# Performance work log

Hardware: AMD Instinct MI355X
Metric: run time of the kernel (lower is better)

Reference implementation:

```python
import jax, jax.numpy as jnp
import numpy as np

N_NODES = 50000
N_EDGES = 800000
D = 128
SAME_W = 0.3
CROSS_W = 1.0


def setup_inputs() -> dict:
    key = jax.random.key(0)
    k1, k2, k3, k4, k5 = jax.random.split(key, 5)
    x = jax.random.normal(k1, (N_NODES, D), dtype=jnp.float32)
    edge_index = jax.random.randint(k2, (2, N_EDGES), 0, N_NODES, dtype=jnp.int64)
    edge_weight = jax.random.uniform(k3, (N_EDGES,), dtype=jnp.float32)
    Wr1 = jax.random.normal(k4, (D, D), dtype=jnp.float32) * (1.0 / np.sqrt(D))
    Wr2 = jax.random.normal(k5, (D, D), dtype=jnp.float32) * (1.0 / np.sqrt(D))
    return {"x": x, "edge_index": edge_index, "edge_weight": edge_weight,
            "Wr1": Wr1, "Wr2": Wr2, "cell_len": 20000}


def _node_types(idx, cell_len):
    # get_node_types: type 0 if idx <= cell_len, else 1 (note the <=, faithful to source)
    return (idx > cell_len).astype(jnp.int32)


def _conv_layer(x, src, dst, per_edge_w, Wr, n_nodes):
    # gather -> weight -> scatter-mean -> + root linear
    msg = x[src] * per_edge_w[:, None]                       # [E, D]
    agg = jax.ops.segment_sum(msg, dst, num_segments=n_nodes)  # [N, D]
    cnt = jax.ops.segment_sum(jnp.ones_like(per_edge_w), dst, num_segments=n_nodes)
    agg = agg / jnp.maximum(cnt, 1.0)[:, None]               # mean aggr (0 if no edges)
    return agg + x @ Wr.T                                     # lin_r, bias=False


def reference(x, edge_index, edge_weight, Wr1, Wr2, cell_len):
    src, dst = edge_index[0], edge_index[1]
    same = _node_types(src, cell_len) == _node_types(dst, cell_len)
    type_w = jnp.where(same, SAME_W, CROSS_W).astype(x.dtype)
    w = type_w * edge_weight                                  # [E]
    n_nodes = x.shape[0]
    h = _conv_layer(x, src, dst, w, Wr1, n_nodes)
    out = _conv_layer(h, src, dst, w, Wr2, n_nodes)
    return out
```

## Files before the change

### kernel.cpp

```cpp
#include <hip/hip_runtime.h>
#include <cstdint>
#include <cstddef>

#define D 128
#define SAME_W 0.3f
#define CROSS_W 1.0f
#define NSLICE 8
#define CAP 64
#define GEMM_BLOCKS 1024

using bf16x8 = __attribute__((ext_vector_type(8))) __bf16;
using f32x4  = __attribute__((ext_vector_type(4))) float;
using i32x4  = __attribute__((ext_vector_type(4))) int;

__device__ __forceinline__ unsigned bf16rne(float f) {
    unsigned u = __float_as_uint(f);
    return (u + 0x7FFFu + ((u >> 16) & 1u)) >> 16;
}

__global__ __launch_bounds__(256) void k_pre(
    const int* __restrict__ src, const int* __restrict__ dst,
    const float* __restrict__ ew, const int* __restrict__ cell_len,
    int* __restrict__ cnt, unsigned* __restrict__ meta, int E, int sliceLen,
    int nFill,
    const float* __restrict__ xf, uint2* __restrict__ xh2,
    uint2* __restrict__ xl2, unsigned* __restrict__ xq, int nvec, int nSplit,
    const float* __restrict__ W1, const float* __restrict__ W2,
    unsigned* __restrict__ wsh, unsigned* __restrict__ w12h,
    unsigned* __restrict__ w12l)
{
    const int b = blockIdx.x;
    if (b < nFill) {
        const int slice = b & (NSLICE - 1);
        const int lo = slice * sliceLen, hi = lo + sliceLen;
        const int chunk = b >> 3;
        const int c = *cell_len;
        #pragma unroll
        for (int u = 0; u < 2; ++u) {
            const int e = chunk * 2048 + u * 1024 + (int)threadIdx.x * 4;
            if (e + 3 < E) {
                i32x4 d4 = __builtin_nontemporal_load((const i32x4*)(dst + e));
                i32x4 s4 = __builtin_nontemporal_load((const i32x4*)(src + e));
                f32x4 w4 = __builtin_nontemporal_load((const f32x4*)(ew + e));
                #pragma unroll
                for (int k = 0; k < 4; ++k) {
                    const int d = d4[k];
                    if (d >= lo && d < hi) {
                        const int   s = s4[k];
                        const float w = w4[k];
                        float wt = w * (((s > c) == (d > c)) ? SAME_W : CROSS_W);
                        int pos = atomicAdd(&cnt[d], 1);
                        if (pos < CAP)
                            meta[d * CAP + pos] = (unsigned)s | (bf16rne(wt) << 16);
                    }
                }
            } else {
                for (int k = 0; k < 4; ++k) {
                    const int ee = e + k;
                    if (ee < E) {
                        int d = __builtin_nontemporal_load(&dst[ee]);
                        if (d >= lo && d < hi) {
                            int s = __builtin_nontemporal_load(&src[ee]);
                            float w = __builtin_nontemporal_load(&ew[ee]);
                            float wt = w * (((s > c) == (d > c)) ? SAME_W : CROSS_W);
                            int pos = atomicAdd(&cnt[d], 1);
                            if (pos < CAP)
                                meta[d * CAP + pos] = (unsigned)s | (bf16rne(wt) << 16);
                        }
                    }
                }
            }
        }
    } else if (b < nFill + nSplit) {
        int i = (b - nFill) * 256 + (int)threadIdx.x;
        if (i >= nvec) return;
        const f32x4* px = (const f32x4*)(xf + (size_t)i * 4);
        f32x4 v = __builtin_nontemporal_load(px);
        unsigned h0 = bf16rne(v[0]), h1 = bf16rne(v[1]),
                 h2 = bf16rne(v[2]), h3 = bf16rne(v[3]);
        xh2[i] = make_uint2(h0 | (h1 << 16), h2 | (h3 << 16));
        float r0 = v[0] - __uint_as_float(h0 << 16);
        float r1 = v[1] - __uint_as_float(h1 << 16);
        float r2 = v[2] - __uint_as_float(h2 << 16);
        float r3 = v[3] - __uint_as_float(h3 << 16);
        xl2[i] = make_uint2(bf16rne(r0) | (bf16rne(r1) << 16),
                            bf16rne(r2) | (bf16rne(r3) << 16));
        int q = __builtin_amdgcn_cvt_pk_fp8_f32(v[0], v[1], 0, false);
        q = __builtin_amdgcn_cvt_pk_fp8_f32(v[2], v[3], q, true);
        xq[i] = (unsigned)q;
    } else {
        int t = (b - nFill - nSplit) * 256 + threadIdx.x;
        int j = t >> 6, kp = t & 63;
        int k0 = kp * 2;
        float d0 = 0.f, d1 = 0.f;
        #pragma unroll 4
        for (int m = 0; m < D; ++m) {
            float a = W2[j * D + m];
            d0 = fmaf(a, W1[m * D + k0], d0);
            d1 = fmaf(a, W1[m * D + k0 + 1], d1);
        }
        float s0 = W1[j * D + k0] + W2[j * D + k0];
        float s1 = W1[j * D + k0 + 1] + W2[j * D + k0 + 1];
        wsh[j * 64 + kp] = bf16rne(s0) | (bf16rne(s1) << 16);
        unsigned h0 = bf16rne(d0), h1 = bf16rne(d1);
        w12h[j * 64 + kp] = h0 | (h1 << 16);
        float r0 = d0 - __uint_as_float(h0 << 16);
        float r1 = d1 - __uint_as_float(h1 << 16);
        w12l[j * 64 + kp] = bf16rne(r0) | (bf16rne(r1) << 16);
    }
}

template <bool EMIT_FP8>
__global__ __launch_bounds__(256) void k_agg_fp8(const unsigned* __restrict__ xq32,
                                                 const unsigned* __restrict__ meta,
                                                 const int* __restrict__ cnt,
                                                 uint2* __restrict__ outb2,
                                                 unsigned* __restrict__ outq32,
                                                 int N) {
    int gid = blockIdx.x * blockDim.x + threadIdx.x;
    int wid  = gid >> 6;
    int lane = gid & 63;
    int half = lane >> 5, lh = lane & 31;
    int node = wid * 2 + half;
    bool alive = node < N;
    int nodeC = alive ? node : N - 1;
    const int cn0 = cnt[nodeC];
    int cn = alive ? min(cn0, CAP) : 0;
    int cnW = max(cn, __shfl_xor(cn, 32));
    const unsigned* mrow = meta + (size_t)nodeC * CAP;
    float a0 = 0.f, a1 = 0.f, a2 = 0.f, a3 = 0.f;
    int i = 0;
    #pragma unroll 1
    for (; i + 16 <= cnW; i += 16) {
        uint4 mq[4];
        #pragma unroll
        for (int u2 = 0; u2 < 4; ++u2) mq[u2] = ((const uint4*)mrow)[(i >> 2) + u2];
        unsigned v[16];
        #pragma unroll
        for (int u = 0; u < 16; ++u) {
            unsigned m = ((const unsigned*)mq)[u];
            v[u] = xq32[(size_t)(m & 0xFFFFu) * 32 + lh];
        }
        #pragma unroll
        for (int u = 0; u < 16; ++u) {
            unsigned m = ((const unsigned*)mq)[u];
            bool ok = (i + u) < cn;
            unsigned vv = ok ? v[u] : 0u;
            float wt = ok ? __uint_as_float(m & 0xFFFF0000u) : 0.0f;
            a0 = fmaf(__builtin_amdgcn_cvt_f32_fp8(vv, 0), wt, a0);
            a1 = fmaf(__builtin_amdgcn_cvt_f32_fp8(vv, 1), wt, a1);
            a2 = fmaf(__builtin_amdgcn_cvt_f32_fp8(vv, 2), wt, a2);
            a3 = fmaf(__builtin_amdgcn_cvt_f32_fp8(vv, 3), wt, a3);
        }
    }
    #pragma unroll 1
    for (; i + 4 <= cnW; i += 4) {
        uint4 mq = ((const uint4*)mrow)[i >> 2];
        unsigned v[4];
        #pragma unroll
        for (int u = 0; u < 4; ++u)
            v[u] = xq32[(size_t)(((const unsigned*)&mq)[u] & 0xFFFFu) * 32 + lh];
        #pragma unroll
        for (int u = 0; u < 4; ++u) {
            unsigned m = ((const unsigned*)&mq)[u];
            bool ok = (i + u) < cn;
            unsigned vv = ok ? v[u] : 0u;
            float wt = ok ? __uint_as_float(m & 0xFFFF0000u) : 0.0f;
            a0 = fmaf(__builtin_amdgcn_cvt_f32_fp8(vv, 0), wt, a0);
            a1 = fmaf(__builtin_amdgcn_cvt_f32_fp8(vv, 1), wt, a1);
            a2 = fmaf(__builtin_amdgcn_cvt_f32_fp8(vv, 2), wt, a2);
            a3 = fmaf(__builtin_amdgcn_cvt_f32_fp8(vv, 3), wt, a3);
        }
    }
    for (; i < cnW; ++i) {
        unsigned m = mrow[i];
        unsigned v = xq32[(size_t)(m & 0xFFFFu) * 32 + lh];
        bool ok = i < cn;
        unsigned vv = ok ? v : 0u;
        float wt = ok ? __uint_as_float(m & 0xFFFF0000u) : 0.0f;
        a0 = fmaf(__builtin_amdgcn_cvt_f32_fp8(vv, 0), wt, a0);
        a1 = fmaf(__builtin_amdgcn_cvt_f32_fp8(vv, 1), wt, a1);
        a2 = fmaf(__builtin_amdgcn_cvt_f32_fp8(vv, 2), wt, a2);
        a3 = fmaf(__builtin_amdgcn_cvt_f32_fp8(vv, 3), wt, a3);
    }
    if (alive) {
        const float s = 1.0f / (float)max(cn0, 1);
        float r0 = a0 * s, r1 = a1 * s, r2 = a2 * s, r3 = a3 * s;
        uint2 w;
        w.x = bf16rne(r0) | (bf16rne(r1) << 16);
        w.y = bf16rne(r2) | (bf16rne(r3) << 16);
        outb2[(size_t)node * 32 + lh] = w;
        if (EMIT_FP8) {
            int q = __builtin_amdgcn_cvt_pk_fp8_f32(r0, r1, 0, false);
            q = __builtin_amdgcn_cvt_pk_fp8_f32(r2, r3, q, true);
            outq32[(size_t)node * 32 + lh] = (unsigned)q;
        }
    }
}

__global__ __launch_bounds__(256, 2) void k_gemm2(
    const uint4* __restrict__ xh4, const uint4* __restrict__ xl4,
    const uint4* __restrict__ a1h4,
    const uint2* __restrict__ a1q2,
    const unsigned* __restrict__ meta, const int* __restrict__ cnt,
    const uint4* __restrict__ w12h4, const uint4* __restrict__ w12l4,
    const uint4* __restrict__ wsh4,
    float* __restrict__ fout, int N, int nTiles)
{
    __shared__ float ci[16][132];
    const int t = threadIdx.x;
    const int wave = t >> 6, lane = t & 63;
    const int j0 = wave * 32;
    const int lr = lane & 15;
    const int q  = lane >> 4;
    const int g  = t >> 4;
    const int lq = t & 15;

    union FU { uint4 u; bf16x8 v; };

    FU wA[2][4], wB[2][4], wC[2][4];
    #pragma unroll
    for (int jt = 0; jt < 2; ++jt) {
        const int brow = (j0 + jt * 16 + lr) * 16 + q;
        #pragma unroll
        for (int ks = 0; ks < 4; ++ks) {
            wA[jt][ks].u = w12h4[brow + ks * 4];
            wB[jt][ks].u = w12l4[brow + ks * 4];
            wC[jt][ks].u = wsh4[brow + ks * 4];
        }
    }

#define ACC8(VV, WT) do {                                                      \
    a0 = fmaf(__builtin_amdgcn_cvt_f32_fp8((VV).x, 0), (WT), a0);              \
    a1 = fmaf(__builtin_amdgcn_cvt_f32_fp8((VV).x, 1), (WT), a1);              \
    a2 = fmaf(__builtin_amdgcn_cvt_f32_fp8((VV).x, 2), (WT), a2);              \
    a3 = fmaf(__builtin_amdgcn_cvt_f32_fp8((VV).x, 3), (WT), a3);              \
    a4 = fmaf(__builtin_amdgcn_cvt_f32_fp8((VV).y, 0), (WT), a4);              \
    a5 = fmaf(__builtin_amdgcn_cvt_f32_fp8((VV).y, 1), (WT), a5);              \
    a6 = fmaf(__builtin_amdgcn_cvt_f32_fp8((VV).y, 2), (WT), a6);              \
    a7 = fmaf(__builtin_amdgcn_cvt_f32_fp8((VV).y, 3), (WT), a7);              \
} while (0)

    int tile = blockIdx.x;
    const int step = gridDim.x;
    for (; tile < nTiles; tile += step) {
        {
            int rr2 = tile * 16 + g; if (rr2 > N - 1) rr2 = N - 1;
            const int cn0 = cnt[rr2];
            const int cn = min(cn0, CAP);
            const unsigned* mrow = meta + (size_t)rr2 * CAP;
            float a0 = 0.f, a1 = 0.f, a2 = 0.f, a3 = 0.f;
            float a4 = 0.f, a5 = 0.f, a6 = 0.f, a7 = 0.f;
            int i = 0;
            #pragma unroll 1
            for (; i + 8 <= cn; i += 8) {
                uint4 mq[2];
                #pragma unroll
                for (int u2 = 0; u2 < 2; ++u2)
                    mq[u2] = ((const uint4*)mrow)[(i >> 2) + u2];
                uint2 v[8];
                #pragma unroll
                for (int u = 0; u < 8; ++u) {
                    unsigned m = ((const unsigned*)mq)[u];
                    v[u] = a1q2[(size_t)(m & 0xFFFFu) * 16 + lq];
                }
                #pragma unroll
                for (int u = 0; u < 8; ++u) {
                    float wt = __uint_as_float(((const unsigned*)mq)[u] & 0xFFFF0000u);
                    ACC8(v[u], wt);
                }
            }
            for (; i < cn; ++i) {
                unsigned m = mrow[i];
                uint2 v = a1q2[(size_t)(m & 0xFFFFu) * 16 + lq];
                float wt = __uint_as_float(m & 0xFFFF0000u);
                ACC8(v, wt);
            }
            const float s = 1.0f / (float)max(cn0, 1);
            ci[g][lq * 8 + 0] = a0 * s; ci[g][lq * 8 + 1] = a1 * s;
            ci[g][lq * 8 + 2] = a2 * s; ci[g][lq * 8 + 3] = a3 * s;
            ci[g][lq * 8 + 4] = a4 * s; ci[g][lq * 8 + 5] = a5 * s;
            ci[g][lq * 8 + 6] = a6 * s; ci[g][lq * 8 + 7] = a7 * s;
        }
        FU Axh[4], Axl[4], Aa1[4];
        {
            int row_ = tile * 16 + lr; if (row_ > N - 1) row_ = N - 1;
            const int ar_ = row_ * 16 + q;
            #pragma unroll
            for (int ks = 0; ks < 4; ++ks) {
                Axh[ks].u = xh4[ar_ + ks * 4];
                Axl[ks].u = xl4[ar_ + ks * 4];
                Aa1[ks].u = a1h4[ar_ + ks * 4];
            }
        }
        __syncthreads();
        {
            f32x4 c_[2];
            #pragma unroll
            for (int jt = 0; jt < 2; ++jt)
                #pragma unroll
                for (int r = 0; r < 4; ++r)
                    c_[jt][r] = ci[q * 4 + r][j0 + jt * 16 + lr];
            #pragma unroll
            for (int jt = 0; jt < 2; ++jt)
                #pragma unroll
                for (int ks = 0; ks < 4; ++ks) {
                    c_[jt] = __builtin_amdgcn_mfma_f32_16x16x32_bf16(Axh[ks].v, wA[jt][ks].v, c_[jt], 0, 0, 0);
                    c_[jt] = __builtin_amdgcn_mfma_f32_16x16x32_bf16(Axl[ks].v, wA[jt][ks].v, c_[jt], 0, 0, 0);
                    c_[jt] = __builtin_amdgcn_mfma_f32_16x16x32_bf16(Axh[ks].v, wB[jt][ks].v, c_[jt], 0, 0, 0);
                    c_[jt] = __builtin_amdgcn_mfma_f32_16x16x32_bf16(Aa1[ks].v, wC[jt][ks].v, c_[jt], 0, 0, 0);
                }
            #pragma unroll
            for (int jt = 0; jt < 2; ++jt)
                #pragma unroll
                for (int r = 0; r < 4; ++r) {
                    int rr_ = tile * 16 + q * 4 + r;
                    if (rr_ < N)
                        __builtin_nontemporal_store(c_[jt][r],
                            &fout[(size_t)rr_ * D + j0 + jt * 16 + lr]);
                }
        }
        __syncthreads();
    }
#undef ACC8
}

extern "C" void kernel_launch(void* const* d_in, const int* in_sizes, int n_in,
                              void* d_out, int out_size, void* d_ws, size_t ws_size,
                              hipStream_t stream) {
    const float* x        = (const float*)d_in[0];
    const int*   ei       = (const int*)d_in[1];
    const float* ew       = (const float*)d_in[2];
    const float* Wr1      = (const float*)d_in[3];
    const float* Wr2      = (const float*)d_in[4];
    const int*   cell_len = (const int*)d_in[5];

    const int N = in_sizes[0] / D;
    const int E = in_sizes[1] / 2;
    const int* src = ei;
    const int* dst = ei + E;

    char* ws = (char*)d_ws;
    size_t off = 0;
    unsigned* meta = (unsigned*)(ws + off); off += (size_t)4 * CAP * N;
    int*      cnt  = (int*)     (ws + off); off += (size_t)4 * N;
    off = (off + 255) & ~(size_t)255;
    unsigned* xh   = (unsigned*)(ws + off); off += (size_t)2 * N * D;
    unsigned* xl   = (unsigned*)(ws + off); off += (size_t)2 * N * D;
    unsigned* a1h  = (unsigned*)(ws + off); off += (size_t)2 * N * D;
    unsigned* xq   = (unsigned*)(ws + off); off += (size_t)1 * N * D;
    unsigned* a1q  = (unsigned*)(ws + off); off += (size_t)1 * N * D;
    unsigned* wsh  = (unsigned*)(ws + off); off += (size_t)2 * D * D;
    unsigned* w12h = (unsigned*)(ws + off); off += (size_t)2 * D * D;
    unsigned* w12l = (unsigned*)(ws + off); off += (size_t)2 * D * D;
    if (ws_size < off) return;
    float* out = (float*)d_out;

    hipMemsetAsync(cnt, 0, (size_t)4 * N, stream);

    const int sliceLen = (N + NSLICE - 1) / NSLICE;
    const int nFill  = ((E + 2047) / 2048) * NSLICE;
    const int xvec   = N * D / 4;
    const int nSplit = (xvec + 255) / 256;
    const int nW     = (D * 64 + 255) / 256;
    const int aggBlocks = (((N + 1) / 2) * 64 + 255) / 256;
    const int nTiles = (N + 15) / 16;

    k_pre<<<nFill + nSplit + nW, 256, 0, stream>>>(
        src, dst, ew, cell_len, cnt, meta, E, sliceLen, nFill,
        x, (uint2*)xh, (uint2*)xl, xq, xvec, nSplit,
        Wr1, Wr2, wsh, w12h, w12l);

    k_agg_fp8<true><<<aggBlocks, 256, 0, stream>>>(
        xq, meta, cnt, (uint2*)a1h, a1q, N);

    k_gemm2<<<GEMM_BLOCKS, 256, 0, stream>>>((const uint4*)xh, (const uint4*)xl,
                                             (const uint4*)a1h, (const uint2*)a1q,
                                             meta, cnt,
                                             (const uint4*)w12h, (const uint4*)w12l,
                                             (const uint4*)wsh, out, N, nTiles);
}
```

Measured before the change: 228.0 us.

## Software-pipeline next tile's gather with current tile's MFMA in gemm2

Double-buffers the shared aggregation tile and restructures the persistent loop so the next tile's neighbor metadata and first twelve FP8 feature gathers are issued before the current tile's MFMA work, then accumulated afterwards. This aims to hide gather latency behind the matrix multiply and removes one barrier per iteration. The cost is more registers for prefetched values, which may reduce occupancy under the launch bounds. The remaining gather loop past the prefetch also loses the previous 8-way batching.

```diff
diff --git a/kernel.cpp b/kernel.cpp
--- a/kernel.cpp
+++ b/kernel.cpp
@@ -8,6 +8,7 @@
 #define NSLICE 8
 #define CAP 64
 #define GEMM_BLOCKS 1024
+#define PRE 12
 
 using bf16x8 = __attribute__((ext_vector_type(8))) __bf16;
 using f32x4  = __attribute__((ext_vector_type(4))) float;
@@ -207,7 +208,7 @@
     const uint4* __restrict__ wsh4,
     float* __restrict__ fout, int N, int nTiles)
 {
-    __shared__ float ci[16][132];
+    __shared__ float ci[2][16][132];
     const int t = threadIdx.x;
     const int wave = t >> 6, lane = t & 63;
     const int j0 = wave * 32;
@@ -243,45 +244,49 @@
 
     int tile = blockIdx.x;
     const int step = gridDim.x;
+    if (tile >= nTiles) return;
+
+    {
+        int ru = tile * 16 + g; if (ru > N - 1) ru = N - 1;
+        const int cn0 = cnt[ru];
+        const int cn = min(cn0, CAP);
+        const unsigned* mrow = meta + (size_t)ru * CAP;
+        float a0 = 0.f, a1 = 0.f, a2 = 0.f, a3 = 0.f;
+        float a4 = 0.f, a5 = 0.f, a6 = 0.f, a7 = 0.f;
+        for (int i = 0; i < cn; ++i) {
+            unsigned m = mrow[i];
+            uint2 vv = a1q2[(size_t)(m & 0xFFFFu) * 16 + lq];
+            float wt = __uint_as_float(m & 0xFFFF0000u);
+            ACC8(vv, wt);
+        }
+        const float s = 1.0f / (float)max(cn0, 1);
+        ci[0][g][lq * 8 + 0] = a0 * s; ci[0][g][lq * 8 + 1] = a1 * s;
+        ci[0][g][lq * 8 + 2] = a2 * s; ci[0][g][lq * 8 + 3] = a3 * s;
+        ci[0][g][lq * 8 + 4] = a4 * s; ci[0][g][lq * 8 + 5] = a5 * s;
+        ci[0][g][lq * 8 + 6] = a6 * s; ci[0][g][lq * 8 + 7] = a7 * s;
+    }
+    __syncthreads();
+    int cur = 0;
+
     for (; tile < nTiles; tile += step) {
-        {
-            int rr2 = tile * 16 + g; if (rr2 > N - 1) rr2 = N - 1;
-            const int cn0 = cnt[rr2];
-            const int cn = min(cn0, CAP);
-            const unsigned* mrow = meta + (size_t)rr2 * CAP;
-            float a0 = 0.f, a1 = 0.f, a2 = 0.f, a3 = 0.f;
-            float a4 = 0.f, a5 = 0.f, a6 = 0.f, a7 = 0.f;
-            int i = 0;
-            #pragma unroll 1
-            for (; i + 8 <= cn; i += 8) {
-                uint4 mq[2];
-                #pragma unroll
-                for (int u2 = 0; u2 < 2; ++u2)
-                    mq[u2] = ((const uint4*)mrow)[(i >> 2) + u2];
-                uint2 v[8];
-                #pragma unroll
-                for (int u = 0; u < 8; ++u) {
-                    unsigned m = ((const unsigned*)mq)[u];
-                    v[u] = a1q2[(size_t)(m & 0xFFFFu) * 16 + lq];
-                }
-                #pragma unroll
-                for (int u = 0; u < 8; ++u) {
-                    float wt = __uint_as_float(((const unsigned*)mq)[u] & 0xFFFF0000u);
-                    ACC8(v[u], wt);
-                }
-            }
-            for (; i < cn; ++i) {
-                unsigned m = mrow[i];
-                uint2 v = a1q2[(size_t)(m & 0xFFFFu) * 16 + lq];
-                float wt = __uint_as_float(m & 0xFFFF0000u);
-                ACC8(v, wt);
-            }
-            const float s = 1.0f / (float)max(cn0, 1);
-            ci[g][lq * 8 + 0] = a0 * s; ci[g][lq * 8 + 1] = a1 * s;
-            ci[g][lq * 8 + 2] = a2 * s; ci[g][lq * 8 + 3] = a3 * s;
-            ci[g][lq * 8 + 4] = a4 * s; ci[g][lq * 8 + 5] = a5 * s;
-            ci[g][lq * 8 + 6] = a6 * s; ci[g][lq * 8 + 7] = a7 * s;
-        }
+        const int tn = tile + step;
+        const bool hasNext = tn < nTiles;
+
+        int cn0n = 0, cnn = 0, npre = 0;
+        const unsigned* mrown = nullptr;
+        uint4 mq[3];
+        uint2 v[PRE];
+        if (hasNext) {
+            int ru = tn * 16 + g; if (ru > N - 1) ru = N - 1;
+            mrown = meta + (size_t)ru * CAP;
+            cn0n = cnt[ru];
+            mq[0] = ((const uint4*)mrown)[0];
+            mq[1] = ((const uint4*)mrown)[1];
+            mq[2] = ((const uint4*)mrown)[2];
+            cnn = min(cn0n, CAP);
+            npre = min(cnn, PRE);
+        }
+
         FU Axh[4], Axl[4], Aa1[4];
         {
             int row_ = tile * 16 + lr; if (row_ > N - 1) row_ = N - 1;
@@ -293,14 +298,21 @@
                 Aa1[ks].u = a1h4[ar_ + ks * 4];
             }
         }
-        __syncthreads();
+
+        if (hasNext) {
+            #pragma unroll
+            for (int u = 0; u < PRE; ++u)
+                if (u < npre)
+                    v[u] = a1q2[(size_t)(((const unsigned*)mq)[u] & 0xFFFFu) * 16 + lq];
+        }
+
         {
             f32x4 c_[2];
             #pragma unroll
             for (int jt = 0; jt < 2; ++jt)
                 #pragma unroll
                 for (int r = 0; r < 4; ++r)
-                    c_[jt][r] = ci[q * 4 + r][j0 + jt * 16 + lr];
+                    c_[jt][r] = ci[cur][q * 4 + r][j0 + jt * 16 + lr];
             #pragma unroll
             for (int jt = 0; jt < 2; ++jt)
                 #pragma unroll
@@ -320,7 +332,31 @@
                             &fout[(size_t)rr_ * D + j0 + jt * 16 + lr]);
                 }
         }
+
+        if (hasNext) {
+            float a0 = 0.f, a1 = 0.f, a2 = 0.f, a3 = 0.f;
+            float a4 = 0.f, a5 = 0.f, a6 = 0.f, a7 = 0.f;
+            #pragma unroll
+            for (int u = 0; u < PRE; ++u)
+                if (u < npre) {
+                    float wt = __uint_as_float(((const unsigned*)mq)[u] & 0xFFFF0000u);
+                    ACC8(v[u], wt);
+                }
+            for (int i = PRE; i < cnn; ++i) {
+                unsigned m = mrown[i];
+                uint2 vv = a1q2[(size_t)(m & 0xFFFFu) * 16 + lq];
+                float wt = __uint_as_float(m & 0xFFFF0000u);
+                ACC8(vv, wt);
+            }
+            const float s = 1.0f / (float)max(cn0n, 1);
+            const int nb = cur ^ 1;
+            ci[nb][g][lq * 8 + 0] = a0 * s; ci[nb][g][lq * 8 + 1] = a1 * s;
+            ci[nb][g][lq * 8 + 2] = a2 * s; ci[nb][g][lq * 8 + 3] = a3 * s;
+            ci[nb][g][lq * 8 + 4] = a4 * s; ci[nb][g][lq * 8 + 5] = a5 * s;
+            ci[nb][g][lq * 8 + 6] = a6 * s; ci[nb][g][lq * 8 + 7] = a7 * s;
+        }
         __syncthreads();
+        cur ^= 1;
     }
 #undef ACC8
 }
```

After: 254.4 us. 11.6% more time.
